# Optimization experiments

Measured on AMD Instinct MI355X. Metric: run time of the kernel, lower is better.

The kernel has to match this reference:

```python
import jax, jax.numpy as jnp
import numpy as np

B, T, N_EMBD, HEAD = 1024, 256, 384, 64


def setup_inputs() -> dict:
    key = jax.random.key(0)
    kx, kq, kk, kv = jax.random.split(key, 4)
    x = jax.random.normal(kx, (B, T, N_EMBD), dtype=jnp.float32)
    # torch nn.Linear(384, 64, bias=False) weight is [64, 384]; we store the
    # transposed [384, 64] form so forward is x @ W.
    s = 1.0 / np.sqrt(N_EMBD)
    Wq = jax.random.normal(kq, (N_EMBD, HEAD), dtype=jnp.float32) * s
    Wk = jax.random.normal(kk, (N_EMBD, HEAD), dtype=jnp.float32) * s
    Wv = jax.random.normal(kv, (N_EMBD, HEAD), dtype=jnp.float32) * s
    return {"x": x, "Wq": Wq, "Wk": Wk, "Wv": Wv}


def reference(x, Wq, Wk, Wv):
    # Single-head causal self-attention (eval mode: dropout is identity).
    q = jnp.einsum('btn,nh->bth', x, Wq)  # [B,T,H]
    k = jnp.einsum('btn,nh->bth', x, Wk)
    v = jnp.einsum('btn,nh->bth', x, Wv)
    scale = 1.0 / jnp.sqrt(jnp.asarray(HEAD, dtype=x.dtype))
    wei = jnp.einsum('bth,bsh->bts', q, k) * scale  # [B,T,T]
    causal = jnp.tril(jnp.ones((T, T), dtype=bool))
    wei = jnp.where(causal[None, :, :], wei, -jnp.inf)
    wei = jax.nn.softmax(wei, axis=-1)
    out = jnp.einsum('bts,bsh->bth', wei, v)  # [B,T,H]
    return out
```

## Files before the change

kernel.cpp:

```cpp
#include <hip/hip_runtime.h>

#define BB 1024
#define TT 256
#define EE 384
#define HH 64

typedef float  f32x4  __attribute__((ext_vector_type(4)));
typedef float  f32x4v __attribute__((ext_vector_type(4)));
typedef short  short8 __attribute__((ext_vector_type(8)));
typedef unsigned short us4 __attribute__((ext_vector_type(4)));

__device__ __forceinline__ unsigned short f2bf(float f) {
    unsigned int u = __float_as_uint(f);
    u += 0x7FFFu + ((u >> 16) & 1u);
    return (unsigned short)(u >> 16);
}

__global__ void prep_kernel(const float* __restrict__ Wq, const float* __restrict__ Wk,
                            const float* __restrict__ Wv, unsigned short* __restrict__ Wt) {
    int i = blockIdx.x * 256 + threadIdx.x;
    if (i >= 192 * EE) return;
    int n = i / EE, k = i - n * EE;
    float v;
    if (n < 64)       v = Wq[k * HH + n] * 0.18033688011112042f;
    else if (n < 128) v = Wk[k * HH + (n - 64)];
    else              v = Wv[k * HH + (n - 128)];
    Wt[i] = f2bf(v);
}

__global__ __launch_bounds__(512, 2) void attn_kernel(const float* __restrict__ x,
                                                      const unsigned short* __restrict__ Wt,
                                                      float* __restrict__ out) {
    __shared__ unsigned short Qs[TT * 72];
    __shared__ unsigned short Ks[TT * 72];
    __shared__ unsigned short Vt[HH * 264];
    __shared__ unsigned short Ps[8 * 1152];

    const int tid  = threadIdx.x;
    const int lane = tid & 63;
    const int w    = tid >> 6;
    const int g    = lane >> 4;
    const int mr   = lane & 15;
    const int b    = blockIdx.x;
    const float* xb = x + (size_t)b * (TT * EE);

    f32x4 acc[2][12];
#pragma unroll
    for (int ti = 0; ti < 2; ++ti)
#pragma unroll
        for (int nt = 0; nt < 12; ++nt)
            acc[ti][nt] = (f32x4){0.f, 0.f, 0.f, 0.f};

    const int M0a = (2 * w) * 16;
    const int M0b = (2 * w + 1) * 16;

    for (int kt = 0; kt < 12; ++kt) {
        const int k0 = kt * 32 + g * 8;
        short8 bfr[12];
#pragma unroll
        for (int nt = 0; nt < 12; ++nt)
            bfr[nt] = *(const short8*)(Wt + (size_t)(nt * 16 + mr) * EE + k0);
        short8 afr[2];
#pragma unroll
        for (int ti = 0; ti < 2; ++ti) {
            const int m0 = ti ? M0b : M0a;
            const float* ap = xb + (size_t)(m0 + mr) * EE + k0;
            f32x4v lo = *(const f32x4v*)ap;
            f32x4v hi = *(const f32x4v*)(ap + 4);
            union { short8 v; unsigned short u[8]; } cv;
            cv.u[0] = f2bf(lo.x); cv.u[1] = f2bf(lo.y); cv.u[2] = f2bf(lo.z); cv.u[3] = f2bf(lo.w);
            cv.u[4] = f2bf(hi.x); cv.u[5] = f2bf(hi.y); cv.u[6] = f2bf(hi.z); cv.u[7] = f2bf(hi.w);
            afr[ti] = cv.v;
        }
#pragma unroll
        for (int nt = 0; nt < 12; ++nt) {
            acc[0][nt] = __builtin_amdgcn_mfma_f32_16x16x32_bf16(afr[0], bfr[nt], acc[0][nt], 0, 0, 0);
            acc[1][nt] = __builtin_amdgcn_mfma_f32_16x16x32_bf16(afr[1], bfr[nt], acc[1][nt], 0, 0, 0);
        }
    }

#pragma unroll
    for (int ti = 0; ti < 2; ++ti) {
        const int row = (ti ? M0b : M0a) + g * 4;
#pragma unroll
        for (int nt = 0; nt < 12; ++nt) {
            f32x4 v = acc[ti][nt];
            if (nt < 4) {
                const int col = nt * 16 + mr;
#pragma unroll
                for (int r = 0; r < 4; ++r) Qs[(row + r) * 72 + col] = f2bf(v[r]);
            } else if (nt < 8) {
                const int col = (nt - 4) * 16 + mr;
#pragma unroll
                for (int r = 0; r < 4; ++r) Ks[(row + r) * 72 + col] = f2bf(v[r]);
            } else {
                const int h = (nt - 8) * 16 + mr;
                us4 pk;
                pk.x = f2bf(v[0]); pk.y = f2bf(v[1]); pk.z = f2bf(v[2]); pk.w = f2bf(v[3]);
                *(us4*)(&Vt[h * 264 + row]) = pk;
            }
        }
    }
    __syncthreads();

#pragma unroll
    for (int pass = 0; pass < 2; ++pass) {
        const int a  = pass ? (15 - w) : w;
        const int r0 = a * 16;
        f32x4 o[4];
        float mrun[4], lrun[4];
#pragma unroll
        for (int i = 0; i < 4; ++i) {
            o[i] = (f32x4){0.f, 0.f, 0.f, 0.f};
            mrun[i] = -3.0e38f;
            lrun[i] = 0.f;
        }
        const int nch = (a >> 2) + 1;
        unsigned short* pw = Ps + w * 1152;

        for (int j = 0; j < nch; ++j) {
            f32x4 s[4];
#pragma unroll
            for (int nt = 0; nt < 4; ++nt) s[nt] = (f32x4){0.f, 0.f, 0.f, 0.f};
#pragma unroll
            for (int kt = 0; kt < 2; ++kt) {
                short8 qf = *(const short8*)(Qs + (r0 + mr) * 72 + kt * 32 + g * 8);
#pragma unroll
                for (int nt = 0; nt < 4; ++nt) {
                    short8 kf = *(const short8*)(Ks + (j * 64 + nt * 16 + mr) * 72 + kt * 32 + g * 8);
                    s[nt] = __builtin_amdgcn_mfma_f32_16x16x32_bf16(qf, kf, s[nt], 0, 0, 0);
                }
            }
            if (j * 64 + 63 > r0) {
#pragma unroll
                for (int nt = 0; nt < 4; ++nt) {
                    const int key = j * 64 + nt * 16 + mr;
#pragma unroll
                    for (int r = 0; r < 4; ++r) {
                        const int row = r0 + g * 4 + r;
                        if (key > row) s[nt][r] = -3.0e38f;
                    }
                }
            }
            float cm[4];
#pragma unroll
            for (int r = 0; r < 4; ++r) {
                cm[r] = fmaxf(fmaxf(s[0][r], s[1][r]), fmaxf(s[2][r], s[3][r]));
                cm[r] = fmaxf(cm[r], __shfl_xor(cm[r], 1, 64));
                cm[r] = fmaxf(cm[r], __shfl_xor(cm[r], 2, 64));
                cm[r] = fmaxf(cm[r], __shfl_xor(cm[r], 4, 64));
                cm[r] = fmaxf(cm[r], __shfl_xor(cm[r], 8, 64));
            }
            float al[4];
#pragma unroll
            for (int r = 0; r < 4; ++r) {
                float mn = fmaxf(mrun[r], cm[r]);
                al[r] = exp2f(mrun[r] - mn);
                mrun[r] = mn;
            }
            float rs[4] = {0.f, 0.f, 0.f, 0.f};
#pragma unroll
            for (int nt = 0; nt < 4; ++nt) {
#pragma unroll
                for (int r = 0; r < 4; ++r) {
                    float p = exp2f(s[nt][r] - mrun[r]);
                    rs[r] += p;
                    pw[(g * 4 + r) * 72 + nt * 16 + mr] = f2bf(p);
                }
            }
#pragma unroll
            for (int r = 0; r < 4; ++r) {
                rs[r] += __shfl_xor(rs[r], 1, 64);
                rs[r] += __shfl_xor(rs[r], 2, 64);
                rs[r] += __shfl_xor(rs[r], 4, 64);
                rs[r] += __shfl_xor(rs[r], 8, 64);
                lrun[r] = lrun[r] * al[r] + rs[r];
            }
#pragma unroll
            for (int hn = 0; hn < 4; ++hn)
#pragma unroll
                for (int r = 0; r < 4; ++r) o[hn][r] *= al[r];
#pragma unroll
            for (int kt = 0; kt < 2; ++kt) {
                short8 pf = *(const short8*)(pw + mr * 72 + kt * 32 + g * 8);
#pragma unroll
                for (int hn = 0; hn < 4; ++hn) {
                    short8 vf = *(const short8*)(Vt + (hn * 16 + mr) * 264 + j * 64 + kt * 32 + g * 8);
                    o[hn] = __builtin_amdgcn_mfma_f32_16x16x32_bf16(pf, vf, o[hn], 0, 0, 0);
                }
            }
        }
        float* ob = out + ((size_t)b * TT + r0) * HH;
#pragma unroll
        for (int r = 0; r < 4; ++r) {
            const float inv = 1.0f / lrun[r];
#pragma unroll
            for (int hn = 0; hn < 4; ++hn)
                ob[(g * 4 + r) * HH + hn * 16 + mr] = o[hn][r] * inv;
        }
    }
}

extern "C" void kernel_launch(void* const* d_in, const int* in_sizes, int n_in,
                              void* d_out, int out_size, void* d_ws, size_t ws_size,
                              hipStream_t stream) {
    const float* x  = (const float*)d_in[0];
    const float* Wq = (const float*)d_in[1];
    const float* Wk = (const float*)d_in[2];
    const float* Wv = (const float*)d_in[3];
    unsigned short* Wt = (unsigned short*)d_ws;
    float* out = (float*)d_out;

    prep_kernel<<<288, 256, 0, stream>>>(Wq, Wk, Wv, Wt);
    attn_kernel<<<BB, 512, 0, stream>>>(x, Wt, out);
}
```

Before: 654.1 us.

## Split fused attention into separate QKV projection and attention kernels

The single fused kernel becomes two kernels. A QKV projection kernel stages x and pre-swizzled bf16 weights into LDS via global_load_lds and writes bf16 Q/K/V images to workspace. An attention kernel then loads K and V into swizzled LDS, keeps Q in registers, and computes the softmax row sum with an MFMA against a ones vector. The aim is better occupancy in the attention stage (launch bounds 512,4) and LDS-tiled projection without bank conflicts. The cost is a round trip of about 100MB of intermediates through global memory, and the new path only runs if the workspace is large enough, otherwise it falls back to the old kernels.

```diff
diff --git a/kernel.cpp b/kernel.cpp
--- a/kernel.cpp
+++ b/kernel.cpp
@@ -6,7 +6,6 @@
 #define HH 64
 
 typedef float  f32x4  __attribute__((ext_vector_type(4)));
-typedef float  f32x4v __attribute__((ext_vector_type(4)));
 typedef short  short8 __attribute__((ext_vector_type(8)));
 typedef unsigned short us4 __attribute__((ext_vector_type(4)));
 
@@ -15,6 +14,263 @@
     u += 0x7FFFu + ((u >> 16) & 1u);
     return (unsigned short)(u >> 16);
 }
+
+__device__ __forceinline__ void gl_lds16(const void* g, void* l) {
+    __builtin_amdgcn_global_load_lds(
+        (const __attribute__((address_space(1))) unsigned int*)g,
+        (__attribute__((address_space(3))) unsigned int*)l, 16, 0, 0);
+}
+
+
+__global__ void prep2_kernel(const float* __restrict__ Wq, const float* __restrict__ Wk,
+                             const float* __restrict__ Wv, unsigned short* __restrict__ Wt2) {
+    int i = blockIdx.x * 256 + threadIdx.x;
+    if (i >= 12 * 6144) return;
+    int kt = i / 6144;
+    int r1 = i - kt * 6144;
+    int n  = r1 >> 5;
+    int r2 = r1 & 31;
+    int sc = r2 >> 3, e = r2 & 7;
+    int c  = sc ^ (n & 3);
+    int k  = kt * 32 + c * 8 + e;
+    float v;
+    if (n < 64)       v = Wq[k * HH + n] * 0.18033688011112042f;
+    else if (n < 128) v = Wk[k * HH + (n - 64)];
+    else              v = Wv[k * HH + (n - 128)];
+    Wt2[i] = f2bf(v);
+}
+
+__global__ __launch_bounds__(256, 2) void qkv_kernel(const float* __restrict__ x,
+                                                     const unsigned short* __restrict__ Wt2,
+                                                     unsigned short* __restrict__ Qimg,
+                                                     unsigned short* __restrict__ Kimg,
+                                                     unsigned short* __restrict__ Vimg) {
+    __shared__ __align__(16) float          xs[128 * 32];
+    __shared__ __align__(16) unsigned short wts[6144];
+
+    const int tid  = threadIdx.x;
+    const int lane = tid & 63;
+    const int w    = tid >> 6;
+    const int g    = lane >> 4;
+    const int mr   = lane & 15;
+    const int m7   = mr & 7;
+    const int m3   = mr & 3;
+    const long rows0 = (long)blockIdx.x * 128;
+
+    f32x4 acc[2][12];
+#pragma unroll
+    for (int ti = 0; ti < 2; ++ti)
+#pragma unroll
+        for (int nt = 0; nt < 12; ++nt) acc[ti][nt] = (f32x4){0.f, 0.f, 0.f, 0.f};
+
+    const int swb = (g ^ m3) << 3;
+
+    for (int kt = 0; kt < 12; ++kt) {
+        __syncthreads();
+#pragma unroll
+        for (int j = 0; j < 4; ++j) {
+            int chunk = j * 256 + tid;
+            int r = chunk >> 3, c = chunk & 7;
+            const float* src = x + (rows0 + r) * EE + kt * 32 + ((c ^ (r & 7)) << 2);
+            gl_lds16(src, xs + (j * 256 + w * 64) * 4);
+        }
+#pragma unroll
+        for (int j = 0; j < 3; ++j) {
+            int ch = j * 256 + tid;
+            gl_lds16(Wt2 + kt * 6144 + ch * 8, wts + (j * 256 + w * 64) * 8);
+        }
+        __syncthreads();
+
+        short8 afr[2];
+#pragma unroll
+        for (int ti = 0; ti < 2; ++ti) {
+            const int lr = w * 32 + ti * 16 + mr;
+            const float* base = xs + lr * 32;
+            f32x4 lo = *(const f32x4*)(base + (((2 * g)     ^ m7) << 2));
+            f32x4 hi = *(const f32x4*)(base + (((2 * g + 1) ^ m7) << 2));
+            union { short8 v; unsigned short u[8]; } cv;
+            cv.u[0] = f2bf(lo.x); cv.u[1] = f2bf(lo.y); cv.u[2] = f2bf(lo.z); cv.u[3] = f2bf(lo.w);
+            cv.u[4] = f2bf(hi.x); cv.u[5] = f2bf(hi.y); cv.u[6] = f2bf(hi.z); cv.u[7] = f2bf(hi.w);
+            afr[ti] = cv.v;
+        }
+#pragma unroll
+        for (int nt = 0; nt < 12; ++nt) {
+            short8 bfr = *(const short8*)(wts + (nt * 16 + mr) * 32 + swb);
+            acc[0][nt] = __builtin_amdgcn_mfma_f32_16x16x32_bf16(afr[0], bfr, acc[0][nt], 0, 0, 0);
+            acc[1][nt] = __builtin_amdgcn_mfma_f32_16x16x32_bf16(afr[1], bfr, acc[1][nt], 0, 0, 0);
+        }
+    }
+
+    const int b  = blockIdx.x >> 1;
+    const int t0 = (blockIdx.x & 1) * 128;
+    unsigned short* Qb = Qimg + (size_t)b * 16384;
+    unsigned short* Kb = Kimg + (size_t)b * 16384;
+    unsigned short* Vb = Vimg + (size_t)b * 16384;
+
+#pragma unroll
+    for (int ti = 0; ti < 2; ++ti) {
+        const int tbase = t0 + w * 32 + ti * 16;
+#pragma unroll
+        for (int nt = 0; nt < 12; ++nt) {
+            f32x4 v = acc[ti][nt];
+            if (nt < 4) {
+                const int h = nt * 16 + mr;
+#pragma unroll
+                for (int r = 0; r < 4; ++r)
+                    Qb[(tbase + g * 4 + r) * 64 + h] = f2bf(v[r]);
+            } else if (nt < 8) {
+                const int hc = (nt - 4) * 2 + (mr >> 3);
+#pragma unroll
+                for (int r = 0; r < 4; ++r) {
+                    const int t = tbase + g * 4 + r;
+                    Kb[t * 64 + ((hc ^ (t & 7)) << 3) + m7] = f2bf(v[r]);
+                }
+            } else {
+                const int h  = (nt - 8) * 16 + mr;
+                const int tq = tbase + g * 4;
+                const int sw = (tq >> 3) ^ m7;
+                us4 pk;
+                pk.x = f2bf(v[0]); pk.y = f2bf(v[1]); pk.z = f2bf(v[2]); pk.w = f2bf(v[3]);
+                *(us4*)(Vb + h * 256 + sw * 8 + (tq & 7)) = pk;
+            }
+        }
+    }
+}
+
+__global__ __launch_bounds__(512, 4) void attn2_kernel(const unsigned short* __restrict__ Qimg,
+                                                       const unsigned short* __restrict__ Kimg,
+                                                       const unsigned short* __restrict__ Vimg,
+                                                       float* __restrict__ out) {
+    __shared__ __align__(16) unsigned short Ks[16384];
+    __shared__ __align__(16) unsigned short Vs[16384];
+    __shared__ __align__(16) unsigned short Ps[8192];
+
+    const int tid  = threadIdx.x;
+    const int lane = tid & 63;
+    const int w    = tid >> 6;
+    const int g    = lane >> 4;
+    const int mr   = lane & 15;
+    const int m7   = mr & 7;
+    const int b    = blockIdx.x;
+
+    const unsigned short* Qb = Qimg + (size_t)b * 16384;
+    const unsigned short* Kb = Kimg + (size_t)b * 16384;
+    const unsigned short* Vb = Vimg + (size_t)b * 16384;
+
+    short8 qfr[2][2];
+#pragma unroll
+    for (int p = 0; p < 2; ++p) {
+        const int t0 = (w + p * 8) * 16;
+#pragma unroll
+        for (int kt = 0; kt < 2; ++kt)
+            qfr[p][kt] = *(const short8*)(Qb + (t0 + mr) * 64 + kt * 32 + g * 8);
+    }
+
+#pragma unroll
+    for (int j = 0; j < 4; ++j) {
+        int ch = j * 512 + tid;
+        gl_lds16(Kb + ch * 8, Ks + (j * 512 + w * 64) * 8);
+    }
+#pragma unroll
+    for (int j = 0; j < 4; ++j) {
+        int ch = j * 512 + tid;
+        gl_lds16(Vb + ch * 8, Vs + (j * 512 + w * 64) * 8);
+    }
+    __syncthreads();
+
+    const int swv0 = ((0 * 4 + g) ^ m7) << 3;
+    const int swv1 = ((1 * 4 + g) ^ m7) << 3;
+    unsigned short* pw = Ps + w * 1024;
+
+    short8 ones;
+#pragma unroll
+    for (int i = 0; i < 8; ++i) ones[i] = (short)0x3F80;
+
+#pragma unroll
+    for (int p = 0; p < 2; ++p) {
+        const int a   = w + p * 8;
+        const int r0  = a * 16;
+        const int nch = (a >> 2) + 1;
+
+        f32x4 o[4];
+        f32x4 ls = (f32x4){0.f, 0.f, 0.f, 0.f};
+        float mrun[4];
+#pragma unroll
+        for (int i = 0; i < 4; ++i) { o[i] = (f32x4){0.f, 0.f, 0.f, 0.f}; mrun[i] = -3.0e38f; }
+
+        for (int j = 0; j < nch; ++j) {
+            f32x4 s[4];
+#pragma unroll
+            for (int nt = 0; nt < 4; ++nt) s[nt] = (f32x4){0.f, 0.f, 0.f, 0.f};
+#pragma unroll
+            for (int kt = 0; kt < 2; ++kt) {
+                const short8 qf = qfr[p][kt];
+                const int swv = kt ? swv1 : swv0;
+#pragma unroll
+                for (int nt = 0; nt < 4; ++nt) {
+                    short8 kf = *(const short8*)(Ks + (j * 64 + nt * 16 + mr) * 64 + swv);
+                    s[nt] = __builtin_amdgcn_mfma_f32_16x16x32_bf16(qf, kf, s[nt], 0, 0, 0);
+                }
+            }
+            if (j == nch - 1) {
+#pragma unroll
+                for (int nt = 0; nt < 4; ++nt) {
+                    const int key = j * 64 + nt * 16 + mr;
+#pragma unroll
+                    for (int r = 0; r < 4; ++r)
+                        if (key > r0 + g * 4 + r) s[nt][r] = -3.0e38f;
+                }
+            }
+            float cm[4], al[4];
+#pragma unroll
+            for (int r = 0; r < 4; ++r) {
+                cm[r] = fmaxf(fmaxf(s[0][r], s[1][r]), fmaxf(s[2][r], s[3][r]));
+                cm[r] = fmaxf(cm[r], __shfl_xor(cm[r], 1, 64));
+                cm[r] = fmaxf(cm[r], __shfl_xor(cm[r], 2, 64));
+                cm[r] = fmaxf(cm[r], __shfl_xor(cm[r], 4, 64));
+                cm[r] = fmaxf(cm[r], __shfl_xor(cm[r], 8, 64));
+                float mn = fmaxf(mrun[r], cm[r]);
+                al[r] = exp2f(mrun[r] - mn);
+                mrun[r] = mn;
+            }
+#pragma unroll
+            for (int nt = 0; nt < 4; ++nt) {
+#pragma unroll
+                for (int r = 0; r < 4; ++r) {
+                    const int lr = g * 4 + r;
+                    const int sw = (nt * 2 + (mr >> 3)) ^ (lr & 7);
+                    pw[lr * 64 + (sw << 3) + m7] = f2bf(exp2f(s[nt][r] - mrun[r]));
+                }
+            }
+#pragma unroll
+            for (int hn = 0; hn < 4; ++hn)
+#pragma unroll
+                for (int r = 0; r < 4; ++r) o[hn][r] *= al[r];
+#pragma unroll
+            for (int r = 0; r < 4; ++r) ls[r] *= al[r];
+#pragma unroll
+            for (int kt = 0; kt < 2; ++kt) {
+                const int swv = kt ? swv1 : swv0;
+                short8 pf = *(const short8*)(pw + mr * 64 + swv);
+#pragma unroll
+                for (int hn = 0; hn < 4; ++hn) {
+                    short8 vf = *(const short8*)(Vs + (hn * 16 + mr) * 256 + j * 64 + swv);
+                    o[hn] = __builtin_amdgcn_mfma_f32_16x16x32_bf16(pf, vf, o[hn], 0, 0, 0);
+                }
+                ls = __builtin_amdgcn_mfma_f32_16x16x32_bf16(pf, ones, ls, 0, 0, 0);
+            }
+        }
+        float* ob = out + ((size_t)b * TT + r0) * HH;
+#pragma unroll
+        for (int r = 0; r < 4; ++r) {
+            const float inv = 1.0f / ls[r];
+#pragma unroll
+            for (int hn = 0; hn < 4; ++hn)
+                ob[(g * 4 + r) * HH + hn * 16 + mr] = o[hn][r] * inv;
+        }
+    }
+}
+
 
 __global__ void prep_kernel(const float* __restrict__ Wq, const float* __restrict__ Wk,
                             const float* __restrict__ Wv, unsigned short* __restrict__ Wt) {
@@ -32,9 +288,9 @@
                                                       const unsigned short* __restrict__ Wt,
                                                       float* __restrict__ out) {
     __shared__ unsigned short Qs[TT * 72];
-    __shared__ unsigned short Ks[TT * 72];
+    __shared__ unsigned short Ksh[TT * 72];
     __shared__ unsigned short Vt[HH * 264];
-    __shared__ unsigned short Ps[8 * 1152];
+    __shared__ unsigned short Psc[8 * 1152];
 
     const int tid  = threadIdx.x;
     const int lane = tid & 63;
@@ -48,11 +304,9 @@
 #pragma unroll
     for (int ti = 0; ti < 2; ++ti)
 #pragma unroll
-        for (int nt = 0; nt < 12; ++nt)
-            acc[ti][nt] = (f32x4){0.f, 0.f, 0.f, 0.f};
-
-    const int M0a = (2 * w) * 16;
-    const int M0b = (2 * w + 1) * 16;
+        for (int nt = 0; nt < 12; ++nt) acc[ti][nt] = (f32x4){0.f, 0.f, 0.f, 0.f};
+
+    const int M0a = (2 * w) * 16, M0b = (2 * w + 1) * 16;
 
     for (int kt = 0; kt < 12; ++kt) {
         const int k0 = kt * 32 + g * 8;
@@ -65,8 +319,8 @@
         for (int ti = 0; ti < 2; ++ti) {
             const int m0 = ti ? M0b : M0a;
             const float* ap = xb + (size_t)(m0 + mr) * EE + k0;
-            f32x4v lo = *(const f32x4v*)ap;
-            f32x4v hi = *(const f32x4v*)(ap + 4);
+            f32x4 lo = *(const f32x4*)ap;
+            f32x4 hi = *(const f32x4*)(ap + 4);
             union { short8 v; unsigned short u[8]; } cv;
             cv.u[0] = f2bf(lo.x); cv.u[1] = f2bf(lo.y); cv.u[2] = f2bf(lo.z); cv.u[3] = f2bf(lo.w);
             cv.u[4] = f2bf(hi.x); cv.u[5] = f2bf(hi.y); cv.u[6] = f2bf(hi.z); cv.u[7] = f2bf(hi.w);
@@ -92,7 +346,7 @@
             } else if (nt < 8) {
                 const int col = (nt - 4) * 16 + mr;
 #pragma unroll
-                for (int r = 0; r < 4; ++r) Ks[(row + r) * 72 + col] = f2bf(v[r]);
+                for (int r = 0; r < 4; ++r) Ksh[(row + r) * 72 + col] = f2bf(v[r]);
             } else {
                 const int h = (nt - 8) * 16 + mr;
                 us4 pk;
@@ -112,11 +366,10 @@
 #pragma unroll
         for (int i = 0; i < 4; ++i) {
             o[i] = (f32x4){0.f, 0.f, 0.f, 0.f};
-            mrun[i] = -3.0e38f;
-            lrun[i] = 0.f;
+            mrun[i] = -3.0e38f; lrun[i] = 0.f;
         }
         const int nch = (a >> 2) + 1;
-        unsigned short* pw = Ps + w * 1152;
+        unsigned short* pwv = Psc + w * 1152;
 
         for (int j = 0; j < nch; ++j) {
             f32x4 s[4];
@@ -127,7 +380,7 @@
                 short8 qf = *(const short8*)(Qs + (r0 + mr) * 72 + kt * 32 + g * 8);
 #pragma unroll
                 for (int nt = 0; nt < 4; ++nt) {
-                    short8 kf = *(const short8*)(Ks + (j * 64 + nt * 16 + mr) * 72 + kt * 32 + g * 8);
+                    short8 kf = *(const short8*)(Ksh + (j * 64 + nt * 16 + mr) * 72 + kt * 32 + g * 8);
                     s[nt] = __builtin_amdgcn_mfma_f32_16x16x32_bf16(qf, kf, s[nt], 0, 0, 0);
                 }
             }
@@ -136,10 +389,8 @@
                 for (int nt = 0; nt < 4; ++nt) {
                     const int key = j * 64 + nt * 16 + mr;
 #pragma unroll
-                    for (int r = 0; r < 4; ++r) {
-                        const int row = r0 + g * 4 + r;
-                        if (key > row) s[nt][r] = -3.0e38f;
-                    }
+                    for (int r = 0; r < 4; ++r)
+                        if (key > r0 + g * 4 + r) s[nt][r] = -3.0e38f;
                 }
             }
             float cm[4];
@@ -163,9 +414,9 @@
             for (int nt = 0; nt < 4; ++nt) {
 #pragma unroll
                 for (int r = 0; r < 4; ++r) {
-                    float p = exp2f(s[nt][r] - mrun[r]);
-                    rs[r] += p;
-                    pw[(g * 4 + r) * 72 + nt * 16 + mr] = f2bf(p);
+                    float pv = exp2f(s[nt][r] - mrun[r]);
+                    rs[r] += pv;
+                    pwv[(g * 4 + r) * 72 + nt * 16 + mr] = f2bf(pv);
                 }
             }
 #pragma unroll
@@ -182,7 +433,7 @@
                 for (int r = 0; r < 4; ++r) o[hn][r] *= al[r];
 #pragma unroll
             for (int kt = 0; kt < 2; ++kt) {
-                short8 pf = *(const short8*)(pw + mr * 72 + kt * 32 + g * 8);
+                short8 pf = *(const short8*)(pwv + mr * 72 + kt * 32 + g * 8);
 #pragma unroll
                 for (int hn = 0; hn < 4; ++hn) {
                     short8 vf = *(const short8*)(Vt + (hn * 16 + mr) * 264 + j * 64 + kt * 32 + g * 8);
@@ -200,6 +451,7 @@
         }
     }
 }
+
 
 extern "C" void kernel_launch(void* const* d_in, const int* in_sizes, int n_in,
                               void* d_out, int out_size, void* d_ws, size_t ws_size,
@@ -208,9 +460,22 @@
     const float* Wq = (const float*)d_in[1];
     const float* Wk = (const float*)d_in[2];
     const float* Wv = (const float*)d_in[3];
-    unsigned short* Wt = (unsigned short*)d_ws;
     float* out = (float*)d_out;
 
-    prep_kernel<<<288, 256, 0, stream>>>(Wq, Wk, Wv, Wt);
-    attn_kernel<<<BB, 512, 0, stream>>>(x, Wt, out);
-}
+    const size_t img = (size_t)1024 * 16384;
+    const size_t need = 147456 + 3 * img * 2;
+
+    if (ws_size >= need) {
+        unsigned short* Wt2  = (unsigned short*)d_ws;
+        unsigned short* Qimg = (unsigned short*)((char*)d_ws + 147456);
+        unsigned short* Kimg = Qimg + img;
+        unsigned short* Vimg = Kimg + img;
+        prep2_kernel<<<288, 256, 0, stream>>>(Wq, Wk, Wv, Wt2);
+        qkv_kernel<<<2048, 256, 0, stream>>>(x, Wt2, Qimg, Kimg, Vimg);
+        attn2_kernel<<<1024, 512, 0, stream>>>(Qimg, Kimg, Vimg, out);
+    } else {
+        unsigned short* Wt = (unsigned short*)d_ws;
+        prep_kernel<<<288, 256, 0, stream>>>(Wq, Wk, Wv, Wt);
+        attn_kernel<<<BB, 512, 0, stream>>>(x, Wt, out);
+    }
+}
```

Result: faster. 605.3 us (-7.5%).
